# Kernel tuning notes

Measured on AMD Instinct MI355X. Metric: run time of the kernel, lower is better.

## Reference

```python
import jax, jax.numpy as jnp
import numpy as np

DIM = 128      # input node feature dim
GS = 64        # SAGEConv output dim
AF = 32        # additional (ir_score) feature dim
NB = 2         # nb_classes
G = 8192       # num_graphs in batch
NPG = 16       # nodes per graph
N = G * NPG    # total nodes = 131072
E = 2097152    # total edges (avg degree 16)


def setup_inputs() -> dict:
    key = jax.random.key(0)
    ks = jax.random.split(key, 10)

    def w(k, shape, fan_in):
        return jax.random.normal(k, shape, jnp.float32) / np.sqrt(fan_in)

    return {
        "x": jax.random.normal(ks[0], (N, DIM), jnp.float32),
        "edge_index": jax.random.randint(ks[1], (2, E), 0, N),
        "set_indices": jax.random.randint(ks[2], (G, 2), 0, NPG),
        "batch_ids": jnp.repeat(jnp.arange(G), NPG),  # sorted graph ids, PyG style
        "ir_score": jax.random.uniform(ks[3], (G, AF), jnp.float32),
        "W_l": w(ks[4], (DIM, GS), DIM),
        "b_l": jnp.zeros((GS,), jnp.float32),
        "W_r": w(ks[5], (DIM, GS), DIM),
        "W_ir": w(ks[6], (AF, 2 * GS), AF),
        "b_ir": jnp.zeros((2 * GS,), jnp.float32),
        "W1": w(ks[7], ((2 * GS) * (2 * GS), 200), (2 * GS) * (2 * GS)),
        "b1": jnp.zeros((200,), jnp.float32),
        "W2": w(ks[8], (200, NB), 200),
        "b2": jnp.zeros((NB,), jnp.float32),
    }


def reference(x, edge_index, set_indices, batch_ids, ir_score,
              W_l, b_l, W_r, W_ir, b_ir, W1, b1, W2, b2):
    n = x.shape[0]
    src, dst = edge_index[0], edge_index[1]

    # SAGEConv (mean aggregation): out = lin_l(mean_{j in N(i)} x_j) + lin_r(x_i)
    agg = jax.ops.segment_sum(x[src], dst, num_segments=n)           # [N, DIM]
    deg = jax.ops.segment_sum(jnp.ones((src.shape[0],), x.dtype), dst, num_segments=n)
    mean = agg / jnp.maximum(deg, 1.0)[:, None]
    h = jax.nn.relu(mean @ W_l + b_l + x @ W_r)                      # [N, GS]

    # per-graph node counts -> index bases (cumsum), then global pair indices
    g = set_indices.shape[0]
    num_nodes = jax.ops.segment_sum(jnp.ones((n,), jnp.float32), batch_ids, num_segments=g)
    csum = jnp.cumsum(num_nodes.astype(jnp.int64))
    index_bases = jnp.concatenate([jnp.zeros((1,), jnp.int64), csum[:-1]])
    sib = index_bases[:, None] + set_indices                         # [G, 2]

    pair = h[sib].reshape(g, 2 * GS)                                 # gather + flatten

    # fusion: relu(linear(ir_score)) then per-graph outer product
    S = jax.nn.relu(ir_score @ W_ir + b_ir)                          # [G, 2*GS]
    outer = jnp.einsum('gi,gj->gij', pair, S).reshape(g, -1)         # [G, (2GS)^2]

    # decode MLP
    z = jax.nn.relu(outer @ W1 + b1)                                 # [G, 200]
    logits = z @ W2 + b2                                             # [G, NB]
    return logits
```

## Files before the change

### kernel.cpp

```cpp
#include <hip/hip_runtime.h>

#define NN   131072
#define GG   8192
#define EE   2097152
#define KBIG 16384
#define NPAD 208
#define NSPLIT 8
#define NSEL  16384
#define SBUCK 256
#define SUBC  4
#define SCAPS 336
#define SCAPT (SUBC*SCAPS)

typedef _Float16 half_t;
typedef __attribute__((ext_vector_type(8))) _Float16 half8;
typedef __attribute__((ext_vector_type(4))) float floatx4;

__device__ inline floatx4 mfma16(half8 a, half8 b, floatx4 c) {
  return __builtin_amdgcn_mfma_f32_16x16x32_f16(a, b, c, 0, 0, 0);
}

__global__ void prep_w(const float* __restrict__ Wl, const float* __restrict__ Wr,
                       half_t* __restrict__ Wt) {
  int idx = blockIdx.x * blockDim.x + threadIdx.x;
  int n = idx >> 7, k = idx & 127;
  float v = (n < 64) ? Wl[k * 64 + n] : Wr[k * 64 + (n - 64)];
  Wt[n * 128 + k] = (half_t)v;
}
__global__ void prep_w1p(const float* __restrict__ W1, half_t* __restrict__ W1p) {
  int idx = blockIdx.x * blockDim.x + threadIdx.x;
  int lane = idx & 63;
  int t = idx >> 6;
  int nt = t % 13; t /= 13;
  int jc = t & 3;  t >>= 2;
  int i  = t & 15; t >>= 4;
  int split = t;
  int n = nt * 16 + (lane & 15);
  int k0 = split * 2048 + i * 128 + jc * 32 + (lane >> 4) * 8;
  half8 v;
#pragma unroll
  for (int e = 0; e < 8; e++)
    v[e] = (half_t)((n < 200) ? W1[(size_t)(k0 + e) * 200 + n] : 0.f);
  *(half8*)(W1p + (size_t)idx * 8) = v;
}

__global__ void set_slots(const int* __restrict__ set_idx, int* __restrict__ nodemap,
                          int* __restrict__ slot_node) {
  int idx = blockIdx.x * blockDim.x + threadIdx.x;
  int g = idx >> 1, which = idx & 1;
  int node = g * 16 + set_idx[g * 2 + which];
  slot_node[idx] = node;
  nodemap[node] = idx;
}

__global__ void filter_scatter(const int* __restrict__ src, const int* __restrict__ dst,
                               const int* __restrict__ nodemap,
                               int* __restrict__ scnt, unsigned int* __restrict__ sbuf) {
  int e = blockIdx.x * blockDim.x + threadIdx.x;
  int d = dst[e];
  int slot = nodemap[d];
  if (slot >= 0) {
    int b = slot >> 6;
    int sub = blockIdx.x & (SUBC - 1);
    int pos = atomicAdd(&scnt[(b * SUBC + sub) * 16], 1);
    if (pos < SCAPS)
      sbuf[(size_t)(b * SUBC + sub) * SCAPS + pos] =
          (unsigned int)src[e] | ((unsigned int)(slot & 63) << 17);
  }
}

__global__ __launch_bounds__(256) void yr_gemm(const float* __restrict__ x,
                                               const half_t* __restrict__ Wt,
                                               const float* __restrict__ b_l,
                                               half_t* __restrict__ y16,
                                               half_t* __restrict__ r16) {
  int tid = threadIdx.x, w = tid >> 6, lane = tid & 63;
  int m = lane & 15, kc = (lane >> 4) * 8;
  int node0 = blockIdx.x * 64 + w * 16;
  floatx4 acc[8];
#pragma unroll
  for (int nt = 0; nt < 8; nt++) acc[nt] = (floatx4){0.f, 0.f, 0.f, 0.f};
#pragma unroll
  for (int step = 0; step < 4; step++) {
    int k0 = step * 32 + kc;
    const float* xp = x + (size_t)(node0 + m) * 128 + k0;
    float4 u0 = *(const float4*)xp;
    float4 u1 = *(const float4*)(xp + 4);
    half8 av = {(half_t)u0.x, (half_t)u0.y, (half_t)u0.z, (half_t)u0.w,
                (half_t)u1.x, (half_t)u1.y, (half_t)u1.z, (half_t)u1.w};
#pragma unroll
    for (int nt = 0; nt < 8; nt++) {
      half8 bv = *(const half8*)(Wt + (nt * 16 + m) * 128 + k0);
      acc[nt] = mfma16(av, bv, acc[nt]);
    }
  }
  int col = lane & 15, rb = (lane >> 4) * 4;
#pragma unroll
  for (int nt = 0; nt < 8; nt++) {
    int n = nt * 16 + col;
    float bias = (n >= 64) ? b_l[n - 64] : 0.f;
#pragma unroll
    for (int r = 0; r < 4; r++) {
      int row = node0 + rb + r;
      float v = acc[nt][r] + bias;
      if (n < 64) y16[(size_t)row * 64 + n] = (half_t)v;
      else        r16[(size_t)row * 64 + (n - 64)] = (half_t)v;
    }
  }
}

__global__ __launch_bounds__(256) void slot_agg(const unsigned int* __restrict__ sbuf,
                                                const int* __restrict__ scnt,
                                                const int* __restrict__ slot_node,
                                                const half_t* __restrict__ y16,
                                                const half_t* __restrict__ r16,
                                                half_t* __restrict__ h_slot) {
  __shared__ int sorted[SCAPT];
  __shared__ int hist[64];
  __shared__ int base[64];
  __shared__ int start[65];
  int b = blockIdx.x, tid = threadIdx.x;
  if (tid < 64) hist[tid] = 0;
  __syncthreads();
  unsigned int myedge[2 * SUBC];
  int mycnt = 0;
#pragma unroll
  for (int sub = 0; sub < SUBC; sub++) {
    int n = scnt[(b * SUBC + sub) * 16]; if (n > SCAPS) n = SCAPS;
    const unsigned int* eb = sbuf + (size_t)(b * SUBC + sub) * SCAPS;
    for (int e = tid; e < n; e += 256) {
      unsigned int pk = eb[e];
      myedge[mycnt++] = pk;
      atomicAdd(&hist[pk >> 17], 1);
    }
  }
  __syncthreads();
  if (tid < 64) {
    int v = hist[tid];
    int sum = v;
#pragma unroll
    for (int off = 1; off < 64; off <<= 1) {
      int u = __shfl_up(sum, off);
      if (tid >= off) sum += u;
    }
    start[tid] = sum - v;
    base[tid]  = sum - v;
    if (tid == 63) start[64] = sum;
  }
  __syncthreads();
  for (int i = 0; i < mycnt; i++) {
    unsigned int pk = myedge[i];
    int pos = atomicAdd(&base[pk >> 17], 1);
    sorted[pos] = (int)(pk & 0x1FFFF);
  }
  __syncthreads();
  int s = tid >> 2, p = tid & 3;
  int e0 = start[s], e1 = start[s + 1];
  float acc[16];
#pragma unroll
  for (int j = 0; j < 16; j++) acc[j] = 0.f;
  int e = e0;
  for (; e + 2 <= e1; e += 2) {
    int s0 = sorted[e], s1 = sorted[e + 1];
    const half8* p0 = (const half8*)(y16 + (size_t)s0 * 64 + p * 16);
    const half8* p1 = (const half8*)(y16 + (size_t)s1 * 64 + p * 16);
    half8 a0 = p0[0], c0 = p0[1], a1 = p1[0], c1 = p1[1];
#pragma unroll
    for (int j = 0; j < 8; j++) {
      acc[j]     += (float)a0[j] + (float)a1[j];
      acc[8 + j] += (float)c0[j] + (float)c1[j];
    }
  }
  if (e < e1) {
    int s0 = sorted[e];
    const half8* p0 = (const half8*)(y16 + (size_t)s0 * 64 + p * 16);
    half8 a0 = p0[0], c0 = p0[1];
#pragma unroll
    for (int j = 0; j < 8; j++) { acc[j] += (float)a0[j]; acc[8 + j] += (float)c0[j]; }
  }
  int slot = b * 64 + s;
  int node = slot_node[slot];
  float inv = 1.0f / fmaxf((float)(e1 - e0), 1.0f);
  const half8* rr = (const half8*)(r16 + (size_t)node * 64 + p * 16);
  half8 r0 = rr[0], r1 = rr[1];
  half8 o0, o1;
#pragma unroll
  for (int j = 0; j < 8; j++) {
    o0[j] = (half_t)fmaxf(acc[j] * inv + (float)r0[j], 0.f);
    o1[j] = (half_t)fmaxf(acc[8 + j] * inv + (float)r1[j], 0.f);
  }
  half8* hp = (half8*)(h_slot + (size_t)slot * 64 + p * 16);
  hp[0] = o0;
  hp[1] = o1;
}

__global__ void s_pair_kernel(const float* __restrict__ ir, const float* __restrict__ W_ir,
                              const float* __restrict__ b_ir, half_t* __restrict__ S16,
                              const half_t* __restrict__ h_slot,
                              const int* __restrict__ nodemap,
                              const int* __restrict__ set_idx, half_t* __restrict__ pair16) {
  int idx = blockIdx.x * blockDim.x + threadIdx.x;
  int g = idx >> 7, o = idx & 127;
  const float* irow = ir + g * 32;
  float sv = b_ir[o];
#pragma unroll
  for (int a = 0; a < 32; a++) sv += irow[a] * W_ir[a * 128 + o];
  S16[idx] = (half_t)fmaxf(sv, 0.f);
  int which = o >> 6, c = o & 63;
  int node = g * 16 + set_idx[g * 2 + which];
  int slot = nodemap[node];
  pair16[idx] = h_slot[(size_t)slot * 64 + c];
}

__global__ __launch_bounds__(256, 1) void biggemm(const half_t* __restrict__ pair16,
                                                  const half_t* __restrict__ S16,
                                                  const half_t* __restrict__ W1p,
                                                  float* __restrict__ zpart) {
  __shared__ half_t bbuf[2][26 * 512];
  __shared__ half_t pls[16][256];
  int bx = blockIdx.x;
  int mt = bx >> 3, split = bx & 7;
  int g0 = mt * 256;
  int tid = threadIdx.x, w = tid >> 6, lane = tid & 63;
  int m = lane & 15, q = lane >> 4, kc = q * 8;

  auto stage = [&](int ii, int halfsel, int bufsel) {
#pragma unroll
    for (int ff = 0; ff < 7; ff++) {
      int f = ff * 4 + w;
      if (f < 26) {
        const half_t* gsrc = W1p + (((size_t)(split * 16 + ii) * 52) + halfsel * 26 + f) * 512 + lane * 8;
        half_t* ldst = &bbuf[bufsel][f * 512];
        __builtin_amdgcn_global_load_lds((const __attribute__((address_space(1))) uint32_t*)gsrc,
                                         (__attribute__((address_space(3))) uint32_t*)ldst, 16, 0, 0);
      }
    }
  };

  stage(0, 0, 0);

  {
    half8 pa = *(const half8*)(pair16 + (size_t)(g0 + tid) * 128 + split * 16);
    half8 pb = *(const half8*)(pair16 + (size_t)(g0 + tid) * 128 + split * 16 + 8);
#pragma unroll
    for (int j = 0; j < 8; j++) { pls[j][tid] = pa[j]; pls[8 + j][tid] = pb[j]; }
  }

  half8 sf[4][4];
#pragma unroll
  for (int sub = 0; sub < 4; sub++) {
    int grow = g0 + w * 64 + sub * 16 + m;
#pragma unroll
    for (int jc = 0; jc < 4; jc++)
      sf[sub][jc] = *(const half8*)(S16 + (size_t)grow * 128 + jc * 32 + kc);
  }

  floatx4 acc[4][13];
#pragma unroll
  for (int sb = 0; sb < 4; sb++)
#pragma unroll
    for (int nt = 0; nt < 13; nt++) acc[sb][nt] = (floatx4){0.f, 0.f, 0.f, 0.f};

  for (int i = 0; i < 16; i++) {
    half_t p0, p1, p2, p3;
#pragma unroll
    for (int h2 = 0; h2 < 2; h2++) {
      __syncthreads();
      if (h2 == 0) {
        p0 = pls[i][w * 64 + 0 * 16 + m];
        p1 = pls[i][w * 64 + 1 * 16 + m];
        p2 = pls[i][w * 64 + 2 * 16 + m];
        p3 = pls[i][w * 64 + 3 * 16 + m];
        stage(i, 1, 1);
      } else if (i < 15) {
        stage(i + 1, 0, 0);
      }
      const half_t* bb = bbuf[h2];
#pragma unroll
      for (int jj = 0; jj < 2; jj++) {
        const int jc = h2 * 2 + jj;
        half8 a0 = sf[0][jc] * p0;
        half8 a1 = sf[1][jc] * p1;
        half8 a2 = sf[2][jc] * p2;
        half8 a3 = sf[3][jc] * p3;
#pragma unroll
        for (int nt = 0; nt < 13; nt++) {
          half8 bv = *(const half8*)(bb + (jj * 13 + nt) * 512 + lane * 8);
          acc[0][nt] = mfma16(a0, bv, acc[0][nt]);
          acc[1][nt] = mfma16(a1, bv, acc[1][nt]);
          acc[2][nt] = mfma16(a2, bv, acc[2][nt]);
          acc[3][nt] = mfma16(a3, bv, acc[3][nt]);
        }
      }
    }
  }

#pragma unroll
  for (int sub = 0; sub < 4; sub++)
#pragma unroll
    for (int nt = 0; nt < 13; nt++)
#pragma unroll
      for (int r = 0; r < 4; r++) {
        int row = g0 + w * 64 + sub * 16 + q * 4 + r;
        zpart[((size_t)split * GG + row) * NPAD + nt * 16 + m] = acc[sub][nt][r];
      }
}

__global__ __launch_bounds__(256) void reduce_mlp(const float* __restrict__ zpart,
                                                  const float* __restrict__ b1,
                                                  const float* __restrict__ W2,
                                                  const float* __restrict__ b2,
                                                  float* __restrict__ out) {
  int tid = threadIdx.x;
  int w = tid >> 6, lane = tid & 63;
  int g = blockIdx.x * 4 + w;
  float p0 = 0.f, p1 = 0.f;
#pragma unroll
  for (int qq = 0; qq < 4; qq++) {
    int c = qq * 64 + lane;
    if (c < 200) {
      float z = 0.f;
#pragma unroll
      for (int sp = 0; sp < NSPLIT; sp++)
        z += zpart[((size_t)sp * GG + g) * NPAD + c];
      z += b1[c];
      z = fmaxf(z, 0.f);
      p0 += z * W2[c * 2];
      p1 += z * W2[c * 2 + 1];
    }
  }
#pragma unroll
  for (int off = 32; off; off >>= 1) {
    p0 += __shfl_down(p0, off);
    p1 += __shfl_down(p1, off);
  }
  if (lane == 0) {
    out[g * 2] = p0 + b2[0];
    out[g * 2 + 1] = p1 + b2[1];
  }
}

extern "C" void kernel_launch(void* const* d_in, const int* in_sizes, int n_in,
                              void* d_out, int out_size, void* d_ws, size_t ws_size,
                              hipStream_t stream) {
  const float* x     = (const float*)d_in[0];
  const int*   ei    = (const int*)d_in[1];
  const int*   setix = (const int*)d_in[2];
  const float* ir    = (const float*)d_in[4];
  const float* W_l   = (const float*)d_in[5];
  const float* b_l   = (const float*)d_in[6];
  const float* W_r   = (const float*)d_in[7];
  const float* W_ir  = (const float*)d_in[8];
  const float* b_ir  = (const float*)d_in[9];
  const float* W1    = (const float*)d_in[10];
  const float* b1    = (const float*)d_in[11];
  const float* W2    = (const float*)d_in[12];
  const float* b2    = (const float*)d_in[13];
  float* out = (float*)d_out;

  char* ws = (char*)d_ws;
  size_t off = 0;
  auto alloc = [&](size_t bytes) -> void* {
    void* p = ws + off;
    off = (off + bytes + 255) & ~(size_t)255;
    return p;
  };
  size_t pool_start = off;
  int* nodemap   = (int*)alloc((size_t)NN * 4);
  int* slot_node = (int*)alloc((size_t)NSEL * 4);
  int* scnt      = (int*)alloc((size_t)SBUCK * SUBC * 16 * 4);
  unsigned int* sbuf = (unsigned int*)alloc((size_t)SBUCK * SUBC * SCAPS * 4);
  half_t* y16    = (half_t*)alloc((size_t)NN * 64 * 2);
  half_t* r16    = (half_t*)alloc((size_t)NN * 64 * 2);
  half_t* h_slot = (half_t*)alloc((size_t)NSEL * 64 * 2);
  float* zpart = (float*)(ws + pool_start);
  {
    size_t zend = pool_start + (((size_t)NSPLIT * GG * NPAD * 4 + 255) & ~(size_t)255);
    if (off < zend) off = zend;
  }
  half_t* Wt     = (half_t*)alloc(128 * 128 * 2);
  half_t* W1p    = (half_t*)alloc((size_t)NPAD * KBIG * 2);
  half_t* S16    = (half_t*)alloc((size_t)GG * 128 * 2);
  half_t* pair16 = (half_t*)alloc((size_t)GG * 128 * 2);
  (void)ws_size; (void)in_sizes; (void)n_in; (void)out_size;

  const int* esrc = ei;
  const int* edst = ei + EE;

  hipMemsetAsync(nodemap, 0xFF, (size_t)NN * 4, stream);
  hipMemsetAsync(scnt, 0, (size_t)SBUCK * SUBC * 16 * 4, stream);

  prep_w<<<(128 * 128) / 256, 256, 0, stream>>>(W_l, W_r, Wt);
  prep_w1p<<<(NPAD * KBIG / 8) / 256, 256, 0, stream>>>(W1, W1p);

  set_slots<<<NSEL / 256, 256, 0, stream>>>(setix, nodemap, slot_node);
  filter_scatter<<<EE / 256, 256, 0, stream>>>(esrc, edst, nodemap, scnt, sbuf);

  yr_gemm<<<NN / 64, 256, 0, stream>>>(x, Wt, b_l, y16, r16);
  slot_agg<<<SBUCK, 256, 0, stream>>>(sbuf, scnt, slot_node, y16, r16, h_slot);

  s_pair_kernel<<<(GG * 128) / 256, 256, 0, stream>>>(ir, W_ir, b_ir, S16, h_slot, nodemap, setix, pair16);

  biggemm<<<(GG / 256) * NSPLIT, 256, 0, stream>>>(pair16, S16, W1p, zpart);
  reduce_mlp<<<GG / 4, 256, 0, stream>>>(zpart, b1, W2, b2, out);
}
```

Baseline: 307.0 us.

## Switch outer-product GEMM to 32x32x16 MFMA with direct global B loads

Rewrites the big outer-product GEMM to use 32x32x16 f16 MFMA tiles, with W1 repacked into a matching 32-column layout padded to 224 columns. The LDS double-buffered staging and barriers are dropped; each wave loads its two B column tiles straight from global/L2, and pair values are read directly. Blocks now cover 128 graphs instead of 256, doubling the grid. The aim is higher MFMA throughput per instruction and more occupancy without sync overhead, at the cost of redundant global B reads across waves and wider zpart rows.

```diff
diff --git a/kernel.cpp b/kernel.cpp
--- a/kernel.cpp
+++ b/kernel.cpp
@@ -4,7 +4,8 @@
 #define GG   8192
 #define EE   2097152
 #define KBIG 16384
-#define NPAD 208
+#define NP2  224
+#define NT2  7
 #define NSPLIT 8
 #define NSEL  16384
 #define SBUCK 256
@@ -15,9 +16,13 @@
 typedef _Float16 half_t;
 typedef __attribute__((ext_vector_type(8))) _Float16 half8;
 typedef __attribute__((ext_vector_type(4))) float floatx4;
+typedef __attribute__((ext_vector_type(16))) float floatx16;
 
 __device__ inline floatx4 mfma16(half8 a, half8 b, floatx4 c) {
   return __builtin_amdgcn_mfma_f32_16x16x32_f16(a, b, c, 0, 0, 0);
+}
+__device__ inline floatx16 mfma32(half8 a, half8 b, floatx16 c) {
+  return __builtin_amdgcn_mfma_f32_32x32x16_f16(a, b, c, 0, 0, 0);
 }
 
 __global__ void prep_w(const float* __restrict__ Wl, const float* __restrict__ Wr,
@@ -27,21 +32,21 @@
   float v = (n < 64) ? Wl[k * 64 + n] : Wr[k * 64 + (n - 64)];
   Wt[n * 128 + k] = (half_t)v;
 }
-__global__ void prep_w1p(const float* __restrict__ W1, half_t* __restrict__ W1p) {
+__global__ void prep_w1q(const float* __restrict__ W1, half_t* __restrict__ W1q) {
   int idx = blockIdx.x * blockDim.x + threadIdx.x;
   int lane = idx & 63;
   int t = idx >> 6;
-  int nt = t % 13; t /= 13;
-  int jc = t & 3;  t >>= 2;
+  int nt = t % 7; t /= 7;
+  int kc = t & 7;  t >>= 3;
   int i  = t & 15; t >>= 4;
   int split = t;
-  int n = nt * 16 + (lane & 15);
-  int k0 = split * 2048 + i * 128 + jc * 32 + (lane >> 4) * 8;
+  int n = nt * 32 + (lane & 31);
+  int k0 = split * 2048 + i * 128 + kc * 16 + (lane >> 5) * 8;
   half8 v;
 #pragma unroll
   for (int e = 0; e < 8; e++)
     v[e] = (half_t)((n < 200) ? W1[(size_t)(k0 + e) * 200 + n] : 0.f);
-  *(half8*)(W1p + (size_t)idx * 8) = v;
+  *(half8*)(W1q + (size_t)idx * 8) = v;
 }
 
 __global__ void set_slots(const int* __restrict__ set_idx, int* __restrict__ nodemap,
@@ -212,98 +217,63 @@
   pair16[idx] = h_slot[(size_t)slot * 64 + c];
 }
 
-__global__ __launch_bounds__(256, 1) void biggemm(const half_t* __restrict__ pair16,
-                                                  const half_t* __restrict__ S16,
-                                                  const half_t* __restrict__ W1p,
-                                                  float* __restrict__ zpart) {
-  __shared__ half_t bbuf[2][26 * 512];
-  __shared__ half_t pls[16][256];
+__global__ __launch_bounds__(256) void biggemm(const half_t* __restrict__ pair16,
+                                               const half_t* __restrict__ S16,
+                                               const half_t* __restrict__ W1q,
+                                               float* __restrict__ zpart) {
   int bx = blockIdx.x;
   int mt = bx >> 3, split = bx & 7;
-  int g0 = mt * 256;
+  int g0 = mt * 128;
   int tid = threadIdx.x, w = tid >> 6, lane = tid & 63;
-  int m = lane & 15, q = lane >> 4, kc = q * 8;
-
-  auto stage = [&](int ii, int halfsel, int bufsel) {
-#pragma unroll
-    for (int ff = 0; ff < 7; ff++) {
-      int f = ff * 4 + w;
-      if (f < 26) {
-        const half_t* gsrc = W1p + (((size_t)(split * 16 + ii) * 52) + halfsel * 26 + f) * 512 + lane * 8;
-        half_t* ldst = &bbuf[bufsel][f * 512];
-        __builtin_amdgcn_global_load_lds((const __attribute__((address_space(1))) uint32_t*)gsrc,
-                                         (__attribute__((address_space(3))) uint32_t*)ldst, 16, 0, 0);
+  int m32 = lane & 31, kh = lane >> 5;
+  int t0 = w;
+  int t1 = (w < 3) ? w + 4 : 3;
+
+  half8 sf[4][8];
+#pragma unroll
+  for (int sub = 0; sub < 4; sub++)
+#pragma unroll
+    for (int kc = 0; kc < 8; kc++)
+      sf[sub][kc] = *(const half8*)(S16 + (size_t)(g0 + sub * 32 + m32) * 128 + kc * 16 + kh * 8);
+
+  const half_t* pp = pair16 + (size_t)(g0 + m32) * 128 + split * 16;
+
+  floatx16 acc0[4], acc1[4];
+#pragma unroll
+  for (int sub = 0; sub < 4; sub++)
+#pragma unroll
+    for (int r = 0; r < 16; r++) { acc0[sub][r] = 0.f; acc1[sub][r] = 0.f; }
+
+  const half8* bq = (const half8*)W1q + (size_t)split * 896 * 64 + lane;
+
+  for (int i = 0; i < 16; i++) {
+    half_t ps[4];
+#pragma unroll
+    for (int sub = 0; sub < 4; sub++)
+      ps[sub] = pp[sub * 4096 + i];
+    const half8* bi = bq + (size_t)(i * 8) * 7 * 64;
+#pragma unroll
+    for (int kc = 0; kc < 8; kc++) {
+      half8 b0 = bi[(kc * 7 + t0) * 64];
+      half8 b1 = bi[(kc * 7 + t1) * 64];
+#pragma unroll
+      for (int sub = 0; sub < 4; sub++) {
+        half8 a = sf[sub][kc] * ps[sub];
+        acc0[sub] = mfma32(a, b0, acc0[sub]);
+        acc1[sub] = mfma32(a, b1, acc1[sub]);
       }
     }
-  };
-
-  stage(0, 0, 0);
-
-  {
-    half8 pa = *(const half8*)(pair16 + (size_t)(g0 + tid) * 128 + split * 16);
-    half8 pb = *(const half8*)(pair16 + (size_t)(g0 + tid) * 128 + split * 16 + 8);
-#pragma unroll
-    for (int j = 0; j < 8; j++) { pls[j][tid] = pa[j]; pls[8 + j][tid] = pb[j]; }
-  }
-
-  half8 sf[4][4];
-#pragma unroll
-  for (int sub = 0; sub < 4; sub++) {
-    int grow = g0 + w * 64 + sub * 16 + m;
-#pragma unroll
-    for (int jc = 0; jc < 4; jc++)
-      sf[sub][jc] = *(const half8*)(S16 + (size_t)grow * 128 + jc * 32 + kc);
-  }
-
-  floatx4 acc[4][13];
-#pragma unroll
-  for (int sb = 0; sb < 4; sb++)
-#pragma unroll
-    for (int nt = 0; nt < 13; nt++) acc[sb][nt] = (floatx4){0.f, 0.f, 0.f, 0.f};
-
-  for (int i = 0; i < 16; i++) {
-    half_t p0, p1, p2, p3;
-#pragma unroll
-    for (int h2 = 0; h2 < 2; h2++) {
-      __syncthreads();
-      if (h2 == 0) {
-        p0 = pls[i][w * 64 + 0 * 16 + m];
-        p1 = pls[i][w * 64 + 1 * 16 + m];
-        p2 = pls[i][w * 64 + 2 * 16 + m];
-        p3 = pls[i][w * 64 + 3 * 16 + m];
-        stage(i, 1, 1);
-      } else if (i < 15) {
-        stage(i + 1, 0, 0);
-      }
-      const half_t* bb = bbuf[h2];
-#pragma unroll
-      for (int jj = 0; jj < 2; jj++) {
-        const int jc = h2 * 2 + jj;
-        half8 a0 = sf[0][jc] * p0;
-        half8 a1 = sf[1][jc] * p1;
-        half8 a2 = sf[2][jc] * p2;
-        half8 a3 = sf[3][jc] * p3;
-#pragma unroll
-        for (int nt = 0; nt < 13; nt++) {
-          half8 bv = *(const half8*)(bb + (jj * 13 + nt) * 512 + lane * 8);
-          acc[0][nt] = mfma16(a0, bv, acc[0][nt]);
-          acc[1][nt] = mfma16(a1, bv, acc[1][nt]);
-          acc[2][nt] = mfma16(a2, bv, acc[2][nt]);
-          acc[3][nt] = mfma16(a3, bv, acc[3][nt]);
-        }
-      }
-    }
   }
 
 #pragma unroll
   for (int sub = 0; sub < 4; sub++)
 #pragma unroll
-    for (int nt = 0; nt < 13; nt++)
-#pragma unroll
-      for (int r = 0; r < 4; r++) {
-        int row = g0 + w * 64 + sub * 16 + q * 4 + r;
-        zpart[((size_t)split * GG + row) * NPAD + nt * 16 + m] = acc[sub][nt][r];
-      }
+    for (int reg = 0; reg < 16; reg++) {
+      int row = g0 + sub * 32 + (reg & 3) + 8 * (reg >> 2) + 4 * kh;
+      size_t base = ((size_t)split * GG + row) * NP2;
+      zpart[base + t0 * 32 + m32] = acc0[sub][reg];
+      if (w < 3) zpart[base + t1 * 32 + m32] = acc1[sub][reg];
+    }
 }
 
 __global__ __launch_bounds__(256) void reduce_mlp(const float* __restrict__ zpart,
@@ -322,7 +292,7 @@
       float z = 0.f;
 #pragma unroll
       for (int sp = 0; sp < NSPLIT; sp++)
-        z += zpart[((size_t)sp * GG + g) * NPAD + c];
+        z += zpart[((size_t)sp * GG + g) * NP2 + c];
       z += b1[c];
       z = fmaxf(z, 0.f);
       p0 += z * W2[c * 2];
@@ -375,11 +345,11 @@
   half_t* h_slot = (half_t*)alloc((size_t)NSEL * 64 * 2);
   float* zpart = (float*)(ws + pool_start);
   {
-    size_t zend = pool_start + (((size_t)NSPLIT * GG * NPAD * 4 + 255) & ~(size_t)255);
+    size_t zend = pool_start + (((size_t)NSPLIT * GG * NP2 * 4 + 255) & ~(size_t)255);
     if (off < zend) off = zend;
   }
   half_t* Wt     = (half_t*)alloc(128 * 128 * 2);
-  half_t* W1p    = (half_t*)alloc((size_t)NPAD * KBIG * 2);
+  half_t* W1q    = (half_t*)alloc((size_t)NSPLIT * 896 * 512 * 2);
   half_t* S16    = (half_t*)alloc((size_t)GG * 128 * 2);
   half_t* pair16 = (half_t*)alloc((size_t)GG * 128 * 2);
   (void)ws_size; (void)in_sizes; (void)n_in; (void)out_size;
@@ -391,7 +361,7 @@
   hipMemsetAsync(scnt, 0, (size_t)SBUCK * SUBC * 16 * 4, stream);
 
   prep_w<<<(128 * 128) / 256, 256, 0, stream>>>(W_l, W_r, Wt);
-  prep_w1p<<<(NPAD * KBIG / 8) / 256, 256, 0, stream>>>(W1, W1p);
+  prep_w1q<<<(NSPLIT * 16 * 8 * 7 * 64) / 256, 256, 0, stream>>>(W1, W1q);
 
   set_slots<<<NSEL / 256, 256, 0, stream>>>(setix, nodemap, slot_node);
   filter_scatter<<<EE / 256, 256, 0, stream>>>(esrc, edst, nodemap, scnt, sbuf);
@@ -401,6 +371,6 @@
 
   s_pair_kernel<<<(GG * 128) / 256, 256, 0, stream>>>(ir, W_ir, b_ir, S16, h_slot, nodemap, setix, pair16);
 
-  biggemm<<<(GG / 256) * NSPLIT, 256, 0, stream>>>(pair16, S16, W1p, zpart);
+  biggemm<<<(GG / 128) * NSPLIT, 256, 0, stream>>>(pair16, S16, W1q, zpart);
   reduce_mlp<<<GG / 4, 256, 0, stream>>>(zpart, b1, W2, b2, out);
 }
```

Result: slower. 355.7 us (+15.8%).
